# Kernel optimization log

Measured on AMD Instinct MI355X. Metric: run time of the kernel, lower is better.

## Reference

```python
import jax, jax.numpy as jnp
import numpy as np

N_NODES = 20000
N_EDGES = 320000
IN_CH = 512
HID = 128
HEADS = 4
OUT_CH = 30
NEG_SLOPE = 0.2  # PyG GATConv default negative_slope


def add_self_loops(ei, n):
    loops = jnp.arange(n, dtype=ei.dtype)
    return jnp.concatenate([ei, jnp.stack([loops, loops])], axis=1)


def gat_layer(x, ei, W, a_src, a_dst, b, concat):
    # x: [N, F_in], ei: [2, E] (source row 0 -> target row 1), W: [F_in, H*C]
    n = x.shape[0]
    H, C = a_src.shape
    h = (x @ W).reshape(n, H, C)                      # [N, H, C]
    src, dst = ei[0], ei[1]
    al_src = jnp.einsum('nhc,hc->nh', h, a_src)       # [N, H]
    al_dst = jnp.einsum('nhc,hc->nh', h, a_dst)
    e = al_src[src] + al_dst[dst]                     # [E, H]
    e = jnp.where(e > 0, e, NEG_SLOPE * e)            # LeakyReLU
    # segment softmax over destination nodes (stable)
    emax = jax.lax.stop_gradient(jax.ops.segment_max(e, dst, num_segments=n))
    p = jnp.exp(e - emax[dst])
    denom = jax.ops.segment_sum(p, dst, num_segments=n)
    alpha = p / denom[dst]                            # [E, H]
    msg = h[src] * alpha[:, :, None]                  # [E, H, C]
    out = jax.ops.segment_sum(msg, dst, num_segments=n)  # [N, H, C]
    out = out.reshape(n, H * C) if concat else out.mean(axis=1)
    return out + b


def setup_inputs() -> dict:
    key = jax.random.key(0)
    ks = jax.random.split(key, 12)
    s = 0.05
    x = jax.random.normal(ks[0], (N_NODES, IN_CH), jnp.float32)
    edge_index = jax.random.randint(ks[1], (2, N_EDGES), 0, N_NODES, jnp.int32)
    return {
        'x': x,
        'edge_index': edge_index,
        'W1': jax.random.normal(ks[2], (IN_CH, HEADS * HID), jnp.float32) * s,
        'a_src1': jax.random.normal(ks[3], (HEADS, HID), jnp.float32) * s,
        'a_dst1': jax.random.normal(ks[4], (HEADS, HID), jnp.float32) * s,
        'b1': jnp.zeros((HEADS * HID,), jnp.float32),
        'W2': jax.random.normal(ks[5], (HEADS * HID, OUT_CH), jnp.float32) * s,
        'a_src2': jax.random.normal(ks[6], (1, OUT_CH), jnp.float32) * s,
        'a_dst2': jax.random.normal(ks[7], (1, OUT_CH), jnp.float32) * s,
        'b2': jnp.zeros((OUT_CH,), jnp.float32),
        'Wd': jax.random.normal(ks[8], (OUT_CH, IN_CH), jnp.float32) * s,
        'bd': jnp.zeros((IN_CH,), jnp.float32),
    }


def reference(x, edge_index, W1, a_src1, a_dst1, b1, W2, a_src2, a_dst2, b2, Wd, bd):
    n = x.shape[0]
    ei = add_self_loops(edge_index, n)
    h = gat_layer(x, ei, W1, a_src1, a_dst1, b1, concat=True)   # [N, HEADS*HID]
    h = jax.nn.elu(h)                                           # dropout is identity in eval
    z = gat_layer(h, ei, W2, a_src2, a_dst2, b2, concat=False)  # [N, OUT_CH]
    x_hat = z @ Wd + bd                                         # [N, IN_CH]
    return (x_hat, z)
```

## Files before the change

### kernel.cpp

```cpp
#include <hip/hip_runtime.h>
#include <hip/hip_bf16.h>
#include <stdint.h>

#define N_NODES 20000
#define N_EDGES 320000
#define IN_CH 512
#define HID 128
#define HEADS 4
#define HC 512
#define OUT_CH 30
#define NEG_SLOPE 0.2f
#define M_PAD 20096
#define PARTS 79
#define CAST_BLOCKS (M_PAD * IN_CH / 4 / 256)
#define G1_BLOCKS (M_PAD / 128 * 4)
#define CNT_BLOCKS (N_EDGES / 256)

typedef _Float16 half8 __attribute__((ext_vector_type(8)));
typedef _Float16 half4v __attribute__((ext_vector_type(4)));
typedef float f32x4 __attribute__((ext_vector_type(4)));

static __device__ __forceinline__ float lrelu(float e) { return e > 0.f ? e : NEG_SLOPE * e; }

static __device__ __forceinline__ void gload16(const void* gsrc, void* ldst) {
  __builtin_amdgcn_global_load_lds(
      (const __attribute__((address_space(1))) uint32_t*)gsrc,
      (__attribute__((address_space(3))) uint32_t*)ldst,
      16, 0, 0);
}

__global__ __launch_bounds__(256) void k_front(const float* __restrict__ x,
                                               const float* __restrict__ W1,
                                               const float* __restrict__ W2,
                                               _Float16* __restrict__ xh,
                                               _Float16* __restrict__ W1t,
                                               _Float16* __restrict__ w2t,
                                               const int* __restrict__ dst,
                                               int* __restrict__ cnt) {
  __shared__ float t[64][65];
  const int b0 = blockIdx.x;
  const int tid = threadIdx.x;
  if (b0 < CNT_BLOCKS) {
    int e = b0 * 256 + tid;
    atomicAdd(&cnt[dst[e]], 1);
    return;
  }
  const int b = b0 - CNT_BLOCKS;
  if (b < CAST_BLOCKS) {
    int i = b * 256 + tid;
    int base = i * 4;
    int row = base >> 9;
    half4v o;
    if (row < N_NODES) {
      float4 v = *(const float4*)(x + (size_t)base);
      o[0] = (_Float16)v.x; o[1] = (_Float16)v.y; o[2] = (_Float16)v.z; o[3] = (_Float16)v.w;
    } else {
      o[0] = o[1] = o[2] = o[3] = (_Float16)0.f;
    }
    *(half4v*)(xh + (size_t)base) = o;
  } else if (b < CAST_BLOCKS + 64) {
    const int bb = b - CAST_BLOCKS;
    const int bk = (bb & 7) * 64;
    const int bn = (bb >> 3) * 64;
#pragma unroll
    for (int it = 0; it < 16; it++) {
      int idx = tid + it * 256;
      int r = idx >> 6, c = idx & 63;
      t[r][c] = W1[(size_t)(bk + r) * HC + bn + c];
    }
    __syncthreads();
#pragma unroll
    for (int it = 0; it < 16; it++) {
      int idx = tid + it * 256;
      int rn = idx >> 6, ck = idx & 63;
      W1t[(size_t)(bn + rn) * IN_CH + bk + ck] = (_Float16)t[ck][rn];
    }
  } else {
    int idx = (b - CAST_BLOCKS - 64) * 256 + tid;
    int n = idx >> 9, k = idx & 511;
    w2t[idx] = (n < OUT_CH) ? (_Float16)W2[(size_t)k * OUT_CH + n] : (_Float16)0.f;
  }
}

__global__ __launch_bounds__(256) void k_gemm1_mfma(const _Float16* __restrict__ A,
                                                    const _Float16* __restrict__ Bt,
                                                    _Float16* __restrict__ C,
                                                    const float* __restrict__ a_src,
                                                    const float* __restrict__ a_dst,
                                                    float* __restrict__ al_s,
                                                    float* __restrict__ al_d) {
  __shared__ _Float16 smem[128 * 136];
  const int bx = blockIdx.x;
  const int tid = threadIdx.x;
  _Float16* As = smem;
  _Float16* Bs = smem + 128 * 64;
  _Float16* Cs = smem;
  const int lane = tid & 63;
  const int w = tid >> 6;
  const int bm = (bx >> 2) * 128;
  const int head = bx & 3;
  const int bn = head * 128;

  const int lrow = lane >> 3;
  const int schunk = (lane & 7) ^ lrow;

  const int wm = w >> 1, wn = w & 1;
  const int r15 = lane & 15;
  const int q = lane >> 4;
  const int a_row0 = wm * 64 + r15;
  const int b_row0 = wn * 64 + r15;

  f32x4 acc[4][4];
  const f32x4 zero = {0.f, 0.f, 0.f, 0.f};
#pragma unroll
  for (int i = 0; i < 4; i++)
#pragma unroll
    for (int j = 0; j < 4; j++) acc[i][j] = zero;

  for (int kb = 0; kb < 8; kb++) {
    const int kof = kb * 64 + schunk * 8;
#pragma unroll
    for (int t = 0; t < 4; t++) {
      const int row = w * 32 + t * 8;
      gload16(A + (size_t)(bm + row + lrow) * IN_CH + kof, (void*)(As + row * 64));
      gload16(Bt + (size_t)(bn + row + lrow) * IN_CH + kof, (void*)(Bs + row * 64));
    }
    __syncthreads();
#pragma unroll
    for (int s = 0; s < 2; s++) {
      const int cs = ((s * 4 + q) ^ (lane & 7)) * 8;
      half8 af[4], bf[4];
#pragma unroll
      for (int i = 0; i < 4; i++) af[i] = *(const half8*)&As[(a_row0 + i * 16) * 64 + cs];
#pragma unroll
      for (int j = 0; j < 4; j++) bf[j] = *(const half8*)&Bs[(b_row0 + j * 16) * 64 + cs];
#pragma unroll
      for (int i = 0; i < 4; i++)
#pragma unroll
        for (int j = 0; j < 4; j++)
          acc[i][j] = __builtin_amdgcn_mfma_f32_16x16x32_f16(af[i], bf[j], acc[i][j], 0, 0, 0);
    }
    __syncthreads();
  }
#pragma unroll
  for (int i = 0; i < 4; i++)
#pragma unroll
    for (int j = 0; j < 4; j++)
#pragma unroll
      for (int r = 0; r < 4; r++) {
        const int row = wm * 64 + i * 16 + q * 4 + r;
        const int col = wn * 64 + j * 16 + r15;
        Cs[row * 136 + col] = (_Float16)acc[i][j][r];
      }
  __syncthreads();
#pragma unroll
  for (int it = 0; it < 8; it++) {
    int cidx = tid + it * 256;
    int row = cidx >> 4, c16 = cidx & 15;
    int gm = bm + row;
    if (gm < N_NODES)
      *(half8*)(C + (size_t)gm * HC + bn + c16 * 8) = *(const half8*)&Cs[row * 136 + c16 * 8];
  }
  const int row = tid >> 1;
  const int hf = tid & 1;
  const float* asp = a_src + head * HID + hf * 64;
  const float* adp = a_dst + head * HID + hf * 64;
  float s = 0.f, d = 0.f;
#pragma unroll
  for (int j8 = 0; j8 < 8; j8++) {
    half8 cv = *(const half8*)&Cs[row * 136 + hf * 64 + j8 * 8];
    float4 a0 = *(const float4*)(asp + j8 * 8);
    float4 a1 = *(const float4*)(asp + j8 * 8 + 4);
    float4 d0 = *(const float4*)(adp + j8 * 8);
    float4 d1 = *(const float4*)(adp + j8 * 8 + 4);
    float c0 = (float)cv[0], c1 = (float)cv[1], c2 = (float)cv[2], c3 = (float)cv[3];
    float c4 = (float)cv[4], c5 = (float)cv[5], c6 = (float)cv[6], c7 = (float)cv[7];
    s += c0 * a0.x + c1 * a0.y + c2 * a0.z + c3 * a0.w +
         c4 * a1.x + c5 * a1.y + c6 * a1.z + c7 * a1.w;
    d += c0 * d0.x + c1 * d0.y + c2 * d0.z + c3 * d0.w +
         c4 * d1.x + c5 * d1.y + c6 * d1.z + c7 * d1.w;
  }
  s += __shfl_xor(s, 1);
  d += __shfl_xor(d, 1);
  const int gm = bm + row;
  if (hf == 0 && gm < N_NODES) {
    al_s[gm * HEADS + head] = s;
    al_d[gm * HEADS + head] = d;
  }
}

__global__ __launch_bounds__(256) void k_scan_part(const int* __restrict__ cnt,
                                                   int* __restrict__ part) {
  __shared__ int ws[4];
  int i = blockIdx.x * 256 + threadIdx.x;
  int v = (i < N_NODES) ? cnt[i] : 0;
  int lane = threadIdx.x & 63;
#pragma unroll
  for (int off = 32; off; off >>= 1) v += __shfl_down(v, off);
  if (lane == 0) ws[threadIdx.x >> 6] = v;
  __syncthreads();
  if (threadIdx.x == 0) part[blockIdx.x] = ws[0] + ws[1] + ws[2] + ws[3];
}
__global__ __launch_bounds__(256) void k_scan_final(const int* __restrict__ cnt,
                                                    const int* __restrict__ part,
                                                    int* __restrict__ offs,
                                                    int* __restrict__ cursor) {
  __shared__ int buf[256];
  __shared__ int s_prefix;
  const int b = blockIdx.x;
  const int t = threadIdx.x;
  if (t < 64) {
    int v = 0;
    for (int j = t; j < b; j += 64) v += part[j];
#pragma unroll
    for (int off = 32; off; off >>= 1) v += __shfl_down(v, off);
    if (t == 0) s_prefix = v;
  }
  int i = b * 256 + t;
  int v = (i < N_NODES) ? cnt[i] : 0;
  buf[t] = v;
  __syncthreads();
#pragma unroll
  for (int off = 1; off < 256; off <<= 1) {
    int x = (t >= off) ? buf[t - off] : 0;
    __syncthreads();
    buf[t] += x;
    __syncthreads();
  }
  if (i < N_NODES) {
    int ex = s_prefix + buf[t] - v;
    offs[i] = ex;
    cursor[i] = ex;
  }
  if (b == PARTS - 1 && t == 255) offs[N_NODES] = s_prefix + buf[255];
}
__global__ void k_scatter(const int* __restrict__ src, const int* __restrict__ dst,
                          int* __restrict__ cursor, int* __restrict__ srcs) {
  int e = blockIdx.x * blockDim.x + threadIdx.x;
  if (e < N_EDGES) {
    int pos = atomicAdd(&cursor[dst[e]], 1);
    srcs[pos] = src[e];
  }
}

__global__ __launch_bounds__(256) void k_agg1(const _Float16* __restrict__ h,
                                              const float* __restrict__ al_s,
                                              const float* __restrict__ al_d,
                                              const int* __restrict__ offs,
                                              const int* __restrict__ srcs,
                                              const float* __restrict__ b1,
                                              _Float16* __restrict__ hm) {
  __shared__ __align__(16) int2 s_sp[4][64];
  const int tid = threadIdx.x;
  const int lane = tid & 63;
  const int wv = tid >> 6;
  const int qq = lane >> 4;
  const int l16 = lane & 15;
  const int head = blockIdx.x / 1250;
  const int n = (blockIdx.x % 1250) * 16 + wv * 4 + qq;
  const int cb = head * HID + l16 * 8;

  const float adn = al_d[n * HEADS + head];
  const float pself = __expf(lrelu(al_s[n * HEADS + head] + adn));

  half8 hv = *(const half8*)(h + (size_t)n * HC + cb);
  float acc[8];
  float den = pself;
#pragma unroll
  for (int j = 0; j < 8; j++) acc[j] = pself * (float)hv[j];

  const int beg = offs[n];
  const int cnt = offs[n + 1] - beg;
  int mx = cnt;
  mx = max(mx, __shfl_xor(mx, 16));
  mx = max(mx, __shfl_xor(mx, 32));

  for (int base = 0; base < mx; base += 16) {
    int sreg = n;
    float preg = 0.f;
    if (base + l16 < cnt) {
      sreg = srcs[beg + base + l16];
      preg = __expf(lrelu(al_s[sreg * HEADS + head] + adn));
    }
    s_sp[wv][lane] = make_int2(sreg, __float_as_int(preg));
    __builtin_amdgcn_wave_barrier();
    const int rem = cnt - base;
    const int m4 = rem > 16 ? 16 : ((rem + 3) & ~3);
    for (int k = 0; k < m4; k += 4) {
      int4 w0 = *(const int4*)&s_sp[wv][qq * 16 + k];
      int4 w1 = *(const int4*)&s_sp[wv][qq * 16 + k + 2];
      half8 v0 = *(const half8*)(h + (size_t)w0.x * HC + cb);
      half8 v1 = *(const half8*)(h + (size_t)w0.z * HC + cb);
      half8 v2 = *(const half8*)(h + (size_t)w1.x * HC + cb);
      half8 v3 = *(const half8*)(h + (size_t)w1.z * HC + cb);
      float p0 = __int_as_float(w0.y), p1 = __int_as_float(w0.w);
      float p2 = __int_as_float(w1.y), p3 = __int_as_float(w1.w);
      den += p0 + p1 + p2 + p3;
#pragma unroll
      for (int j = 0; j < 8; j++)
        acc[j] += p0 * (float)v0[j] + p1 * (float)v1[j] +
                  p2 * (float)v2[j] + p3 * (float)v3[j];
    }
    __builtin_amdgcn_wave_barrier();
  }
  const float inv = 1.f / den;
  float4 bb0 = *(const float4*)(b1 + cb);
  float4 bb1 = *(const float4*)(b1 + cb + 4);
  float ob[8] = {bb0.x, bb0.y, bb0.z, bb0.w, bb1.x, bb1.y, bb1.z, bb1.w};
  half8 ov;
#pragma unroll
  for (int j = 0; j < 8; j++) {
    float o = acc[j] * inv + ob[j];
    o = o > 0.f ? o : __expf(o) - 1.f;
    ov[j] = (_Float16)o;
  }
  *(half8*)(hm + (size_t)n * HC + cb) = ov;
}

__global__ __launch_bounds__(256) void k_gemm2_mfma(const _Float16* __restrict__ hm,
                                                    const _Float16* __restrict__ w2t,
                                                    const float* __restrict__ a_s2,
                                                    const float* __restrict__ a_d2,
                                                    float* __restrict__ zpre,
                                                    float* __restrict__ al_s2,
                                                    float* __restrict__ al_d2) {
  __shared__ _Float16 Bs[32 * 520];
  __shared__ _Float16 As[64 * 136];
  const int tid = threadIdx.x;
  const int lane = tid & 63;
  const int w = tid >> 6;
  const int bm = blockIdx.x * 64;
  const int n15 = lane & 15;
  const int q = lane >> 4;

#pragma unroll
  for (int it = 0; it < 8; it++) {
    int idx = (tid + it * 256) * 8;
    int n = idx >> 9, k = idx & 511;
    *(half8*)&Bs[n * 520 + k] = *(const half8*)(w2t + idx);
  }

  f32x4 acc0 = {0.f, 0.f, 0.f, 0.f}, acc1 = {0.f, 0.f, 0.f, 0.f};
  for (int kt = 0; kt < HC; kt += 128) {
#pragma unroll
    for (int p = 0; p < 4; p++) {
      int row = (tid >> 4) + p * 16;
      int kof = (tid & 15) * 8;
      int gm = bm + row;
      half8 v = {};
      if (gm < N_NODES) v = *(const half8*)(hm + (size_t)gm * HC + kt + kof);
      *(half8*)&As[row * 136 + kof] = v;
    }
    __syncthreads();
#pragma unroll
    for (int ks = 0; ks < 128; ks += 32) {
      half8 af = *(const half8*)&As[(w * 16 + n15) * 136 + ks + q * 8];
      half8 b0 = *(const half8*)&Bs[n15 * 520 + kt + ks + q * 8];
      half8 b1 = *(const half8*)&Bs[(16 + n15) * 520 + kt + ks + q * 8];
      acc0 = __builtin_amdgcn_mfma_f32_16x16x32_f16(af, b0, acc0, 0, 0, 0);
      acc1 = __builtin_amdgcn_mfma_f32_16x16x32_f16(af, b1, acc1, 0, 0, 0);
    }
    __syncthreads();
  }
  const float asn0 = (n15 < OUT_CH) ? a_s2[n15] : 0.f;
  const float asn1 = (n15 + 16 < OUT_CH) ? a_s2[n15 + 16] : 0.f;
  const float adn0 = (n15 < OUT_CH) ? a_d2[n15] : 0.f;
  const float adn1 = (n15 + 16 < OUT_CH) ? a_d2[n15 + 16] : 0.f;
#pragma unroll
  for (int r = 0; r < 4; r++) {
    const int gm = bm + w * 16 + q * 4 + r;
    const bool ok = gm < N_NODES;
    if (ok) {
      zpre[(size_t)gm * OUT_CH + n15] = acc0[r];
      if (n15 + 16 < OUT_CH) zpre[(size_t)gm * OUT_CH + n15 + 16] = acc1[r];
    }
    float s = acc0[r] * asn0 + acc1[r] * asn1;
    float d = acc0[r] * adn0 + acc1[r] * adn1;
#pragma unroll
    for (int off = 8; off; off >>= 1) {
      s += __shfl_xor(s, off);
      d += __shfl_xor(d, off);
    }
    if (n15 == 0 && ok) {
      al_s2[gm] = s;
      al_d2[gm] = d;
    }
  }
}

__global__ __launch_bounds__(256) void k_agg2(const float* __restrict__ zpre,
                                              const float* __restrict__ al_s2,
                                              const float* __restrict__ al_d2,
                                              const int* __restrict__ offs,
                                              const int* __restrict__ srcs,
                                              const float* __restrict__ b2,
                                              float* __restrict__ zout) {
  __shared__ __align__(16) int2 s_sp[4][64];
  const int tid = threadIdx.x;
  const int lane = tid & 63;
  const int wv = tid >> 6;
  const int hh = lane >> 5;
  const int l32 = lane & 31;
  const int n = blockIdx.x * 8 + wv * 2 + hh;
  const float ad2n = al_d2[n];
  const float pself = __expf(lrelu(al_s2[n] + ad2n));
  const bool act = l32 < OUT_CH;
  float zv = act ? zpre[(size_t)n * OUT_CH + l32] : 0.f;
  float acc = pself * zv;
  float den = pself;

  const int beg = offs[n];
  const int cnt = offs[n + 1] - beg;
  int mx = max(cnt, __shfl_xor(cnt, 32));

  for (int base = 0; base < mx; base += 32) {
    int sreg = n;
    float preg = 0.f;
    if (base + l32 < cnt) {
      sreg = srcs[beg + base + l32];
      preg = __expf(lrelu(al_s2[sreg] + ad2n));
    }
    s_sp[wv][lane] = make_int2(sreg, __float_as_int(preg));
    __builtin_amdgcn_wave_barrier();
    const int rem = cnt - base;
    const int m4 = rem > 32 ? 32 : ((rem + 3) & ~3);
    for (int k = 0; k < m4; k += 4) {
      int4 w0 = *(const int4*)&s_sp[wv][hh * 32 + k];
      int4 w1 = *(const int4*)&s_sp[wv][hh * 32 + k + 2];
      float v0 = act ? zpre[(size_t)w0.x * OUT_CH + l32] : 0.f;
      float v1 = act ? zpre[(size_t)w0.z * OUT_CH + l32] : 0.f;
      float v2 = act ? zpre[(size_t)w1.x * OUT_CH + l32] : 0.f;
      float v3 = act ? zpre[(size_t)w1.z * OUT_CH + l32] : 0.f;
      float p0 = __int_as_float(w0.y), p1 = __int_as_float(w0.w);
      float p2 = __int_as_float(w1.y), p3 = __int_as_float(w1.w);
      den += p0 + p1 + p2 + p3;
      acc += p0 * v0 + p1 * v1 + p2 * v2 + p3 * v3;
    }
    __builtin_amdgcn_wave_barrier();
  }
  if (act) zout[(size_t)n * OUT_CH + l32] = acc / den + b2[l32];
}

__global__ __launch_bounds__(256) void k_dec(const float* __restrict__ z,
                                             const float* __restrict__ Wd,
                                             const float* __restrict__ bd,
                                             float* __restrict__ xhat) {
  __shared__ float zs[64][32];
  const int tid = threadIdx.x;
  const int c = blockIdx.y * 256 + tid;
  float wd[32];
#pragma unroll
  for (int k = 0; k < OUT_CH; k++) wd[k] = Wd[(size_t)k * IN_CH + c];
  wd[30] = wd[31] = 0.f;
  const int n0 = blockIdx.x * 64;
  for (int idx = tid; idx < 64 * 32; idx += 256) {
    int r = idx >> 5, cc = idx & 31;
    int row = n0 + r;
    zs[r][cc] = (cc < OUT_CH && row < N_NODES) ? z[(size_t)row * OUT_CH + cc] : 0.f;
  }
  __syncthreads();
  const float b0 = bd[c];
  for (int i = 0; i < 64; i++) {
    int row = n0 + i;
    if (row >= N_NODES) break;
    float a0 = b0;
#pragma unroll
    for (int k4 = 0; k4 < 8; k4++) {
      float4 zv = *(const float4*)&zs[i][k4 * 4];
      a0 += zv.x * wd[k4 * 4 + 0] + zv.y * wd[k4 * 4 + 1] +
            zv.z * wd[k4 * 4 + 2] + zv.w * wd[k4 * 4 + 3];
    }
    xhat[(size_t)row * IN_CH + c] = a0;
  }
}

extern "C" void kernel_launch(void* const* d_in, const int* in_sizes, int n_in,
                              void* d_out, int out_size, void* d_ws, size_t ws_size,
                              hipStream_t stream) {
  const float* x    = (const float*)d_in[0];
  const int*   ei   = (const int*)d_in[1];
  const float* W1   = (const float*)d_in[2];
  const float* a_s1 = (const float*)d_in[3];
  const float* a_d1 = (const float*)d_in[4];
  const float* b1   = (const float*)d_in[5];
  const float* W2   = (const float*)d_in[6];
  const float* a_s2 = (const float*)d_in[7];
  const float* a_d2 = (const float*)d_in[8];
  const float* b2   = (const float*)d_in[9];
  const float* Wd   = (const float*)d_in[10];
  const float* bd   = (const float*)d_in[11];

  float* xhat = (float*)d_out;
  float* zout = xhat + (size_t)N_NODES * IN_CH;

  const int* srcv = ei;
  const int* dstv = ei + N_EDGES;

  char* w = (char*)d_ws;
  auto alloc = [&](size_t bytes) {
    void* p = (void*)w;
    w += (bytes + 255) & ~(size_t)255;
    return p;
  };
  _Float16* xh   = (_Float16*)alloc((size_t)M_PAD * IN_CH * 2);
  _Float16* w1t  = (_Float16*)alloc((size_t)HC * IN_CH * 2);
  _Float16* w2t  = (_Float16*)alloc((size_t)32 * HC * 2);
  _Float16* h    = (_Float16*)alloc((size_t)N_NODES * HC * 2);
  _Float16* hm   = (_Float16*)alloc((size_t)N_NODES * HC * 2);
  float* zpre  = (float*)alloc((size_t)N_NODES * OUT_CH * 4);
  float* al_s1v= (float*)alloc((size_t)N_NODES * HEADS * 4);
  float* al_d1v= (float*)alloc((size_t)N_NODES * HEADS * 4);
  float* al_s2v= (float*)alloc((size_t)N_NODES * 4);
  float* al_d2v= (float*)alloc((size_t)N_NODES * 4);
  int*   cnt   = (int*)alloc((size_t)N_NODES * 4);
  int*   offs  = (int*)alloc((size_t)(N_NODES + 1) * 4);
  int*   cursor= (int*)alloc((size_t)N_NODES * 4);
  int*   srcs  = (int*)alloc((size_t)N_EDGES * 4);
  int*   part  = (int*)alloc((size_t)PARTS * 4);

  const int EB = (N_EDGES + 255) / 256;

  hipMemsetAsync(cnt, 0, (size_t)N_NODES * 4, stream);
  k_front<<<CNT_BLOCKS + CAST_BLOCKS + 128, 256, 0, stream>>>(x, W1, W2, xh, w1t, w2t,
                                                              dstv, cnt);
  k_gemm1_mfma<<<G1_BLOCKS, 256, 0, stream>>>(xh, w1t, h, a_s1, a_d1, al_s1v, al_d1v);
  k_scan_part<<<PARTS, 256, 0, stream>>>(cnt, part);
  k_scan_final<<<PARTS, 256, 0, stream>>>(cnt, part, offs, cursor);
  k_scatter<<<EB, 256, 0, stream>>>(srcv, dstv, cursor, srcs);
  k_agg1<<<1250 * HEADS, 256, 0, stream>>>(h, al_s1v, al_d1v, offs, srcs, b1, hm);
  k_gemm2_mfma<<<(N_NODES + 63) / 64, 256, 0, stream>>>(hm, w2t, a_s2, a_d2, zpre,
                                                        al_s2v, al_d2v);
  k_agg2<<<N_NODES / 8, 256, 0, stream>>>(zpre, al_s2v, al_d2v, offs, srcs, b2, zout);
  k_dec<<<dim3((N_NODES + 63) / 64, 2), 256, 0, stream>>>(zout, Wd, bd, xhat);
}
```

Baseline: 262.5 us.

## Remap layer-1 aggregation so one wave handles all heads of a node

The layer-1 aggregation kernel now assigns one wavefront per destination node covering all four heads (16 lanes per head, 8 channels each), instead of one head of four different nodes per wave. Each neighbor's full 1 KB row of h is read contiguously by the wave, and the edge list and source offsets are loaded once per node rather than once per head. This gives better coalescing, fewer repeated index and offset loads, and no divergence between nodes with different degrees inside a wave. In exchange, waves for high-degree nodes do serial work, and the per-edge probabilities move to a [16][4] shared array.

```diff
diff --git a/kernel.cpp b/kernel.cpp
--- a/kernel.cpp
+++ b/kernel.cpp
@@ -250,15 +250,15 @@
                                               const int* __restrict__ srcs,
                                               const float* __restrict__ b1,
                                               _Float16* __restrict__ hm) {
-  __shared__ __align__(16) int2 s_sp[4][64];
+  __shared__ __align__(16) int s_src[4][16];
+  __shared__ float s_p[4][16][4];
   const int tid = threadIdx.x;
   const int lane = tid & 63;
   const int wv = tid >> 6;
-  const int qq = lane >> 4;
+  const int head = lane >> 4;
   const int l16 = lane & 15;
-  const int head = blockIdx.x / 1250;
-  const int n = (blockIdx.x % 1250) * 16 + wv * 4 + qq;
-  const int cb = head * HID + l16 * 8;
+  const int n = blockIdx.x * 4 + wv;
+  const int cb = lane * 8;
 
   const float adn = al_d[n * HEADS + head];
   const float pself = __expf(lrelu(al_s[n * HEADS + head] + adn));
@@ -271,30 +271,30 @@
 
   const int beg = offs[n];
   const int cnt = offs[n + 1] - beg;
-  int mx = cnt;
-  mx = max(mx, __shfl_xor(mx, 16));
-  mx = max(mx, __shfl_xor(mx, 32));
-
-  for (int base = 0; base < mx; base += 16) {
-    int sreg = n;
+
+  for (int base = 0; base < cnt; base += 16) {
+    int soff = n * HC;
     float preg = 0.f;
     if (base + l16 < cnt) {
-      sreg = srcs[beg + base + l16];
+      int sreg = srcs[beg + base + l16];
+      soff = sreg * HC;
       preg = __expf(lrelu(al_s[sreg * HEADS + head] + adn));
     }
-    s_sp[wv][lane] = make_int2(sreg, __float_as_int(preg));
+    if (head == 0) s_src[wv][l16] = soff;
+    s_p[wv][l16][head] = preg;
     __builtin_amdgcn_wave_barrier();
     const int rem = cnt - base;
     const int m4 = rem > 16 ? 16 : ((rem + 3) & ~3);
     for (int k = 0; k < m4; k += 4) {
-      int4 w0 = *(const int4*)&s_sp[wv][qq * 16 + k];
-      int4 w1 = *(const int4*)&s_sp[wv][qq * 16 + k + 2];
-      half8 v0 = *(const half8*)(h + (size_t)w0.x * HC + cb);
-      half8 v1 = *(const half8*)(h + (size_t)w0.z * HC + cb);
-      half8 v2 = *(const half8*)(h + (size_t)w1.x * HC + cb);
-      half8 v3 = *(const half8*)(h + (size_t)w1.z * HC + cb);
-      float p0 = __int_as_float(w0.y), p1 = __int_as_float(w0.w);
-      float p2 = __int_as_float(w1.y), p3 = __int_as_float(w1.w);
+      int4 s4 = *(const int4*)&s_src[wv][k];
+      float p0 = s_p[wv][k + 0][head];
+      float p1 = s_p[wv][k + 1][head];
+      float p2 = s_p[wv][k + 2][head];
+      float p3 = s_p[wv][k + 3][head];
+      half8 v0 = *(const half8*)(h + (size_t)(s4.x + cb));
+      half8 v1 = *(const half8*)(h + (size_t)(s4.y + cb));
+      half8 v2 = *(const half8*)(h + (size_t)(s4.z + cb));
+      half8 v3 = *(const half8*)(h + (size_t)(s4.w + cb));
       den += p0 + p1 + p2 + p3;
 #pragma unroll
       for (int j = 0; j < 8; j++)
@@ -527,7 +527,7 @@
   k_scan_part<<<PARTS, 256, 0, stream>>>(cnt, part);
   k_scan_final<<<PARTS, 256, 0, stream>>>(cnt, part, offs, cursor);
   k_scatter<<<EB, 256, 0, stream>>>(srcv, dstv, cursor, srcs);
-  k_agg1<<<1250 * HEADS, 256, 0, stream>>>(h, al_s1v, al_d1v, offs, srcs, b1, hm);
+  k_agg1<<<N_NODES / 4, 256, 0, stream>>>(h, al_s1v, al_d1v, offs, srcs, b1, hm);
   k_gemm2_mfma<<<(N_NODES + 63) / 64, 256, 0, stream>>>(hm, w2t, a_s2, a_d2, zpre,
                                                         al_s2v, al_d2v);
   k_agg2<<<N_NODES / 8, 256, 0, stream>>>(zpre, al_s2v, al_d2v, offs, srcs, b2, zout);
```

After: 271.5 us. 3.4% more time.
